# Optimization experiments

Hardware: AMD Instinct MI355X
Metric: run time of the kernel (lower is better)

The kernel has to match this reference:

```python
import jax, jax.numpy as jnp
import numpy as np

DIM = 512
H = 8
HS = DIM // H
SCALES = [25, 12, 7]
ATTN_SCALE = HS ** -0.5
EPS = 1e-5


def _ln(x, g, b):
    m = jnp.mean(x, axis=-1, keepdims=True)
    v = jnp.mean((x - m) ** 2, axis=-1, keepdims=True)
    return (x - m) * jax.lax.rsqrt(v + EPS) * g + b


def setup_inputs() -> dict:
    key = jax.random.key(0)
    ks = jax.random.split(key, 12)
    B, T, J, C = 64, 64, 25, DIM
    w = lambda k, s: jax.random.normal(k, s, dtype=jnp.float32) * 0.02
    return {
        "src": jax.random.normal(ks[0], (B, T, J, C), dtype=jnp.float32),
        "spatial_relation": jax.random.normal(ks[1], (B, T, J, J, 2), dtype=jnp.float32),
        "ln1_g": jnp.ones((C,), jnp.float32),
        "ln1_b": jnp.zeros((C,), jnp.float32),
        "Wq": w(ks[2], (3, C, C)),
        "Wk": w(ks[3], (3, C, C)),
        "Wv": w(ks[4], (3, C, C)),
        "pool0_fc1_w": w(ks[5], (C, 2 * C)),
        "pool0_fc1_b": jnp.zeros((2 * C,), jnp.float32),
        "pool0_fc2_w": w(ks[6], (2 * C, SCALES[1])),
        "pool0_fc2_b": jnp.zeros((SCALES[1],), jnp.float32),
        "pool1_fc1_w": w(ks[7], (C, 2 * C)),
        "pool1_fc1_b": jnp.zeros((2 * C,), jnp.float32),
        "pool1_fc2_w": w(ks[8], (2 * C, SCALES[2])),
        "pool1_fc2_b": jnp.zeros((SCALES[2],), jnp.float32),
    }


def reference(src, spatial_relation, ln1_g, ln1_b, Wq, Wk, Wv,
              pool0_fc1_w, pool0_fc1_b, pool0_fc2_w, pool0_fc2_b,
              pool1_fc1_w, pool1_fc1_b, pool1_fc2_w, pool1_fc2_b):
    # NOTE: in the original torch module, the relation-bias terms (R_qk, R_conv,
    # attn_R_qurt) and spatial_relation_emb are computed but never added to the
    # attention logits, so they do not affect the output; faithful output math below.
    B, T, J, C = src.shape
    x = src.reshape(B * T, J, C)
    g_feat = x  # global (query) features, stay at J nodes
    l_feat = x  # local (key/value) features, get pooled
    pools = [
        (pool0_fc1_w, pool0_fc1_b, pool0_fc2_w, pool0_fc2_b),
        (pool1_fc1_w, pool1_fc1_b, pool1_fc2_w, pool1_fc2_b),
    ]
    outs = []
    for i in range(len(SCALES)):
        qn = _ln(g_feat, ln1_g, ln1_b)
        kn = _ln(l_feat, ln1_g, ln1_b)
        q = (qn @ Wq[i]).reshape(B * T, J, H, HS)
        k = (kn @ Wk[i]).reshape(B * T, -1, H, HS)
        v = (kn @ Wv[i]).reshape(B * T, -1, H, HS)
        logits = jnp.einsum('bnhd,bmhd->bhnm', q, k) * ATTN_SCALE
        a = jax.nn.softmax(logits, axis=-1)
        o = jnp.einsum('bhnm,bmhd->bnhd', a, v).reshape(B * T, J, C)
        outs.append(g_feat + o)
        if i < len(SCALES) - 1:
            f1w, f1b, f2w, f2b = pools[i]
            h = jax.nn.gelu(l_feat @ f1w + f1b, approximate=False)
            S = jax.nn.softmax(h @ f2w + f2b, axis=-1)  # (BT, Ni, Ni+1)
            l_feat = jnp.einsum('bns,bnc->bsc', S, l_feat)
    return jnp.mean(jnp.stack(outs, axis=-1), axis=-1)
```

## Files before the change

kernel.cpp:

```cpp
#include <hip/hip_runtime.h>

typedef unsigned short u16;
typedef unsigned int   u32;
typedef _Float16 f16;
typedef __attribute__((ext_vector_type(8))) unsigned short u16x8;
typedef __attribute__((ext_vector_type(8))) _Float16 f16x8;
typedef __attribute__((ext_vector_type(4))) float f32x4;

__device__ __forceinline__ u16 f2h(float f) {
  f16 h = (f16)f;
  return __builtin_bit_cast(u16, h);
}
__device__ __forceinline__ float h2f(u16 u) {
  return (float)__builtin_bit_cast(f16, u);
}

__global__ __launch_bounds__(256) void prep_w(const float* __restrict__ Wq,
    const float* __restrict__ Wk, const float* __restrict__ Wv,
    const float* __restrict__ f0, const float* __restrict__ f1,
    u16* __restrict__ wt) {
  int t = blockIdx.x * 256 + threadIdx.x;
  float v;
  if (t < 786432) {
    int i = t >> 18, r = t & 262143, n = r >> 9, k = r & 511;
    v = Wq[(size_t)(i << 18) + k * 512 + n];
  } else if (t < 2359296) {
    int r = t - 786432, i = r >> 19, r2 = r & 524287;
    int n = (r2 >> 9) & 511, k = r2 & 511;
    v = ((r2 >> 18) ? Wv : Wk)[(size_t)(i << 18) + k * 512 + n];
  } else if (t < 2883584) {
    int r = t - 2359296, n = r >> 9, k = r & 511;
    v = f0[(size_t)k * 1024 + n];
  } else {
    int r = t - 2883584, n = r >> 9, k = r & 511;
    v = f1[(size_t)k * 1024 + n];
  }
  wt[t] = f2h(v);
}

__global__ __launch_bounds__(256) void ln_f32(const float* __restrict__ x,
    const float* __restrict__ g, const float* __restrict__ bta,
    u16* __restrict__ xn, u16* __restrict__ xb) {
  int row = (blockIdx.x << 2) + (threadIdx.x >> 6);
  int lane = threadIdx.x & 63;
  const float* xr = x + (size_t)row * 512 + (lane << 3);
  float4 a = *(const float4*)xr;
  float4 c = *(const float4*)(xr + 4);
  float v[8] = {a.x, a.y, a.z, a.w, c.x, c.y, c.z, c.w};
  float s = 0.f, s2 = 0.f;
#pragma unroll
  for (int j = 0; j < 8; ++j) { s += v[j]; s2 += v[j] * v[j]; }
  for (int off = 32; off; off >>= 1) { s += __shfl_xor(s, off); s2 += __shfl_xor(s2, off); }
  float mean = s * (1.f / 512.f);
  float var = s2 * (1.f / 512.f) - mean * mean;
  float rs = rsqrtf(var + 1e-5f);
  const float* gp = g + (lane << 3);
  const float* bp = bta + (lane << 3);
  u16x8 pb, pn;
#pragma unroll
  for (int j = 0; j < 8; ++j) {
    pb[j] = f2h(v[j]);
    pn[j] = f2h((v[j] - mean) * rs * gp[j] + bp[j]);
  }
  *(u16x8*)(xb + (size_t)row * 512 + (lane << 3)) = pb;
  *(u16x8*)(xn + (size_t)row * 512 + (lane << 3)) = pn;
}

__global__ __launch_bounds__(256) void ln_b16(const u16* __restrict__ xin,
    const float* __restrict__ g, const float* __restrict__ bta,
    u16* __restrict__ xout) {
  int row = (blockIdx.x << 2) + (threadIdx.x >> 6);
  int lane = threadIdx.x & 63;
  f16x8 u = *(const f16x8*)(xin + (size_t)row * 512 + (lane << 3));
  float v[8];
#pragma unroll
  for (int j = 0; j < 8; ++j) v[j] = (float)u[j];
  float s = 0.f, s2 = 0.f;
#pragma unroll
  for (int j = 0; j < 8; ++j) { s += v[j]; s2 += v[j] * v[j]; }
  for (int off = 32; off; off >>= 1) { s += __shfl_xor(s, off); s2 += __shfl_xor(s2, off); }
  float mean = s * (1.f / 512.f);
  float var = s2 * (1.f / 512.f) - mean * mean;
  float rs = rsqrtf(var + 1e-5f);
  const float* gp = g + (lane << 3);
  const float* bp = bta + (lane << 3);
  u16x8 pn;
#pragma unroll
  for (int j = 0; j < 8; ++j) pn[j] = f2h((v[j] - mean) * rs * gp[j] + bp[j]);
  *(u16x8*)(xout + (size_t)row * 512 + (lane << 3)) = pn;
}

template <bool GELU>
__global__ __launch_bounds__(256, 2) void gemm_bt(const u16* __restrict__ A,
    const u16* __restrict__ Bt, u16* __restrict__ C,
    const float* __restrict__ bias, int M, int N) {
  __shared__ __align__(16) u16 As[128 * 64];
  __shared__ __align__(16) u16 Bs[128 * 64];
  int tid = threadIdx.x;
  int w = tid >> 6, lane = tid & 63;
  int m0 = blockIdx.y << 7, n0 = blockIdx.x << 7;
  int wm = (w & 1) << 6, wn = (w >> 1) << 6;
  f32x4 acc[4][4] = {};
  const int r_off = lane >> 3;
  const int k_off = (lane & 7) << 3;
  for (int kt = 0; kt < 8; ++kt) {
    __syncthreads();
#pragma unroll
    for (int j = 0; j < 4; ++j) {
      int q = (w << 2) + j;
      const u16* gA = A + (size_t)(m0 + (q << 3) + r_off) * 512 + (kt << 6) + k_off;
      __builtin_amdgcn_global_load_lds(
          (const __attribute__((address_space(1))) u32*)gA,
          (__attribute__((address_space(3))) u32*)(As + (q << 9)), 16, 0, 0);
      const u16* gB = Bt + (size_t)(n0 + (q << 3) + r_off) * 512 + (kt << 6) + k_off;
      __builtin_amdgcn_global_load_lds(
          (const __attribute__((address_space(1))) u32*)gB,
          (__attribute__((address_space(3))) u32*)(Bs + (q << 9)), 16, 0, 0);
    }
    asm volatile("s_waitcnt vmcnt(0)" ::: "memory");
    __syncthreads();
#pragma unroll
    for (int kk = 0; kk < 2; ++kk) {
      int ko = (kk << 5) + ((lane >> 4) << 3);
      f16x8 af[4], bfr[4];
#pragma unroll
      for (int mi = 0; mi < 4; ++mi)
        af[mi] = *(const f16x8*)(As + (wm + (mi << 4) + (lane & 15)) * 64 + ko);
#pragma unroll
      for (int ni = 0; ni < 4; ++ni)
        bfr[ni] = *(const f16x8*)(Bs + (wn + (ni << 4) + (lane & 15)) * 64 + ko);
#pragma unroll
      for (int mi = 0; mi < 4; ++mi)
#pragma unroll
        for (int ni = 0; ni < 4; ++ni)
          acc[mi][ni] = __builtin_amdgcn_mfma_f32_16x16x32_f16(af[mi], bfr[ni], acc[mi][ni], 0, 0, 0);
    }
  }
  int cr = (lane >> 4) << 2, cc = lane & 15;
#pragma unroll
  for (int mi = 0; mi < 4; ++mi) {
#pragma unroll
    for (int ni = 0; ni < 4; ++ni) {
      int col = n0 + wn + (ni << 4) + cc;
      float bv = 0.f;
      if (GELU) bv = bias[col];
#pragma unroll
      for (int j = 0; j < 4; ++j) {
        int row = m0 + wm + (mi << 4) + cr + j;
        float v = acc[mi][ni][j];
        if (GELU) { v += bv; v = 0.5f * v * (1.f + erff(v * 0.70710678118f)); }
        C[(size_t)row * N + col] = f2h(v);
      }
    }
  }
}

template <int NKV, bool INIT, int MINW>
__global__ __launch_bounds__(512, MINW) void attn(const u16* __restrict__ Q,
    const u16* __restrict__ KV, const u16* __restrict__ xb, float* __restrict__ out) {
  constexpr int G = 8;
  constexpr int ELEMS = NKV * 1024;
  __shared__ __align__(16) u16 KVl[2][ELEMS];
  int tid = threadIdx.x;
  int b0 = blockIdx.x * G;
  int h = tid >> 6, r = tid & 63, n = r >> 1, half = r & 1;
  int dbase = (h << 6) + (half << 5);
  {
    const u16* src = KV + (size_t)b0 * ELEMS;
    for (int e = tid * 8; e < ELEMS; e += 4096)
      __builtin_amdgcn_global_load_lds(
          (const __attribute__((address_space(1))) u32*)(src + e),
          (__attribute__((address_space(3))) u32*)(KVl[0] + e), 16, 0, 0);
  }
  asm volatile("s_waitcnt vmcnt(0)" ::: "memory");
  __syncthreads();
  for (int t = 0; t < G; ++t) {
    const u16* KVc = KVl[t & 1];
    if (t + 1 < G) {
      const u16* src = KV + (size_t)(b0 + t + 1) * ELEMS;
      u16* dst = KVl[(t + 1) & 1];
      for (int e = tid * 8; e < ELEMS; e += 4096)
        __builtin_amdgcn_global_load_lds(
            (const __attribute__((address_space(1))) u32*)(src + e),
            (__attribute__((address_space(3))) u32*)(dst + e), 16, 0, 0);
    }
    int b = b0 + t;
    if (n < 25) {
      const u16* qr = Q + (size_t)(b * 25 + n) * 512 + dbase;
      f16x8 q8[4];
#pragma unroll
      for (int i = 0; i < 4; ++i) q8[i] = *(const f16x8*)(qr + (i << 3));
      float s[NKV];
      float mx = -1e30f;
#pragma unroll
      for (int m = 0; m < NKV; ++m) {
        const u16* kr = KVc + m * 1024 + dbase;
        float p = 0.f;
#pragma unroll
        for (int i = 0; i < 4; ++i) {
          f16x8 kv = *(const f16x8*)(kr + (i << 3));
#pragma unroll
          for (int j = 0; j < 8; ++j) p += (float)q8[i][j] * (float)kv[j];
        }
        float d = p + __shfl_xor(p, 1);
        s[m] = d * 0.125f;
        mx = fmaxf(mx, s[m]);
      }
      float sum = 0.f;
#pragma unroll
      for (int m = 0; m < NKV; ++m) { s[m] = __expf(s[m] - mx); sum += s[m]; }
      float o[32] = {};
#pragma unroll
      for (int m = 0; m < NKV; ++m) {
        float a = s[m];
        const u16* vr = KVc + m * 1024 + 512 + dbase;
#pragma unroll
        for (int i = 0; i < 4; ++i) {
          f16x8 vv = *(const f16x8*)(vr + (i << 3));
#pragma unroll
          for (int j = 0; j < 8; ++j) o[i * 8 + j] += a * (float)vv[j];
        }
      }
      float sc = (1.f / sum) * (1.f / 3.f);
      float* orow = out + (size_t)(b * 25 + n) * 512 + dbase;
      if (INIT) {
        const u16* xrow = xb + (size_t)(b * 25 + n) * 512 + dbase;
#pragma unroll
        for (int i = 0; i < 4; ++i) {
          f16x8 xv = *(const f16x8*)(xrow + (i << 3));
#pragma unroll
          for (int j = 0; j < 8; j += 4) {
            float4 rr;
            rr.x = o[i * 8 + j + 0] * sc + (float)xv[j + 0];
            rr.y = o[i * 8 + j + 1] * sc + (float)xv[j + 1];
            rr.z = o[i * 8 + j + 2] * sc + (float)xv[j + 2];
            rr.w = o[i * 8 + j + 3] * sc + (float)xv[j + 3];
            *(float4*)(orow + i * 8 + j) = rr;
          }
        }
      } else {
#pragma unroll
        for (int i = 0; i < 8; ++i) {
          float4 pv = *(const float4*)(orow + i * 4);
          float4 rr;
          rr.x = o[i * 4 + 0] * sc + pv.x;
          rr.y = o[i * 4 + 1] * sc + pv.y;
          rr.z = o[i * 4 + 2] * sc + pv.z;
          rr.w = o[i * 4 + 3] * sc + pv.w;
          *(float4*)(orow + i * 4) = rr;
        }
      }
    }
    asm volatile("s_waitcnt vmcnt(0)" ::: "memory");
    __syncthreads();
  }
}

template <int NIN, int NOUT>
__global__ __launch_bounds__(256) void pool(const u16* __restrict__ h,
    const u16* __restrict__ lf, const float* __restrict__ w2,
    const float* __restrict__ b2, u16* __restrict__ lout) {
  __shared__ __align__(16) float W2l[1024 * NOUT];
  __shared__ __align__(16) u16 Xl[NIN * 512];
  __shared__ __align__(16) float Sl[NIN * NOUT];
  int b = blockIdx.x, tid = threadIdx.x;
  for (int e = tid; e < 1024 * NOUT; e += 256) W2l[e] = w2[e];
  for (int e = tid * 8; e < NIN * 512; e += 2048)
    *(u16x8*)(Xl + e) = *(const u16x8*)(lf + (size_t)b * NIN * 512 + e);
  __syncthreads();
  if (tid < NIN * 8) {
    int nn = tid >> 3, sub = tid & 7;
    float p[NOUT] = {};
    const u16* hr = h + (size_t)(b * NIN + nn) * 1024;
    for (int cc = 0; cc < 128; ++cc) {
      int c = sub + (cc << 3);
      float hv = h2f(hr[c]);
#pragma unroll
      for (int s2 = 0; s2 < NOUT; ++s2) p[s2] += hv * W2l[c * NOUT + s2];
    }
#pragma unroll
    for (int s2 = 0; s2 < NOUT; ++s2) {
      p[s2] += __shfl_down(p[s2], 4, 8);
      p[s2] += __shfl_down(p[s2], 2, 8);
      p[s2] += __shfl_down(p[s2], 1, 8);
    }
    if (sub == 0) {
      float mx = -1e30f;
#pragma unroll
      for (int s2 = 0; s2 < NOUT; ++s2) { p[s2] += b2[s2]; mx = fmaxf(mx, p[s2]); }
      float sum = 0.f;
#pragma unroll
      for (int s2 = 0; s2 < NOUT; ++s2) { p[s2] = __expf(p[s2] - mx); sum += p[s2]; }
      float inv = 1.f / sum;
#pragma unroll
      for (int s2 = 0; s2 < NOUT; ++s2) Sl[nn * NOUT + s2] = p[s2] * inv;
    }
  }
  __syncthreads();
  int c0 = tid << 1;
#pragma unroll
  for (int s2 = 0; s2 < NOUT; ++s2) {
    float a0 = 0.f, a1 = 0.f;
#pragma unroll
    for (int nn = 0; nn < NIN; ++nn) {
      float wv = Sl[nn * NOUT + s2];
      a0 += wv * h2f(Xl[nn * 512 + c0]);
      a1 += wv * h2f(Xl[nn * 512 + c0 + 1]);
    }
    u32 pk = (u32)f2h(a0) | ((u32)f2h(a1) << 16);
    *(u32*)(lout + (size_t)(b * NOUT + s2) * 512 + c0) = pk;
  }
}

extern "C" void kernel_launch(void* const* d_in, const int* in_sizes, int n_in,
                              void* d_out, int out_size, void* d_ws, size_t ws_size,
                              hipStream_t stream) {
  const float* src = (const float*)d_in[0];
  const float* g    = (const float*)d_in[2];
  const float* bt   = (const float*)d_in[3];
  const float* Wq   = (const float*)d_in[4];
  const float* Wk   = (const float*)d_in[5];
  const float* Wv   = (const float*)d_in[6];
  const float* f0w  = (const float*)d_in[7];
  const float* f0b  = (const float*)d_in[8];
  const float* f0w2 = (const float*)d_in[9];
  const float* f0b2 = (const float*)d_in[10];
  const float* f1w  = (const float*)d_in[11];
  const float* f1b  = (const float*)d_in[12];
  const float* f1w2 = (const float*)d_in[13];
  const float* f1b2 = (const float*)d_in[14];
  float* out = (float*)d_out;
  char* ws = (char*)d_ws;

  u16* wt  = (u16*)(ws + 0);
  u16* xn  = (u16*)(ws + 6815744);
  u16* xb  = (u16*)(ws + 111673344);
  u16* qb  = (u16*)(ws + 216530944);
  u16* B1  = (u16*)(ws + 321388544);
  u16* l1  = (u16*)(ws + 426246144);
  u16* kn1 = (u16*)(ws + 476577792);
  u16* l2  = qb;
  u16* kn2 = qb + 14680064;

  prep_w<<<13312, 256, 0, stream>>>(Wq, Wk, Wv, f0w, f1w, wt);
  ln_f32<<<25600, 256, 0, stream>>>(src, g, bt, xn, xb);

  gemm_bt<false><<<dim3(4, 800), 256, 0, stream>>>(xn, wt, qb, nullptr, 102400, 512);
  for (int s = 0; s < 2; ++s) {
    size_t ro = (size_t)s * 51200;
    gemm_bt<false><<<dim3(8, 400), 256, 0, stream>>>(xn + ro * 512, wt + 786432, B1, nullptr, 51200, 1024);
    attn<25, true, 1><<<256, 512, 0, stream>>>(qb + ro * 512, B1, xb + ro * 512, out + ro * 512);
  }

  for (int s = 0; s < 2; ++s) {
    size_t ro = (size_t)s * 51200;
    gemm_bt<true><<<dim3(8, 400), 256, 0, stream>>>(xb + ro * 512, wt + 2359296, B1, f0b, 51200, 1024);
    pool<25, 12><<<2048, 256, 0, stream>>>(B1, xb + ro * 512, f0w2, f0b2, l1 + (size_t)s * 2048 * 12 * 512);
  }
  ln_b16<<<12288, 256, 0, stream>>>(l1, g, bt, kn1);

  gemm_bt<false><<<dim3(4, 800), 256, 0, stream>>>(xn, wt + 262144, qb, nullptr, 102400, 512);
  gemm_bt<false><<<dim3(8, 384), 256, 0, stream>>>(kn1, wt + 786432 + 524288, B1, nullptr, 49152, 1024);
  attn<12, false, 2><<<512, 512, 0, stream>>>(qb, B1, nullptr, out);

  gemm_bt<true><<<dim3(8, 384), 256, 0, stream>>>(l1, wt + 2883584, B1, f1b, 49152, 1024);
  pool<12, 7><<<4096, 256, 0, stream>>>(B1, l1, f1w2, f1b2, l2);
  ln_b16<<<7168, 256, 0, stream>>>(l2, g, bt, kn2);

  gemm_bt<false><<<dim3(8, 224), 256, 0, stream>>>(kn2, wt + 786432 + 1048576, B1, nullptr, 28672, 1024);
  gemm_bt<false><<<dim3(4, 800), 256, 0, stream>>>(xn, wt + 524288, qb, nullptr, 102400, 512);
  attn<7, false, 2><<<512, 512, 0, stream>>>(qb, B1, nullptr, out);
}
```

Before: 1.773 ms.

## Use packed fp16 math in attention, fp16 partial sums, swizzle GEMM tiles

The attention QK dot products and PV accumulation now use packed half-precision vector math instead of per-element fp32 FMAs. When the workspace is large enough, the per-scale attention partial sums go to an fp16 scratch buffer rather than a read-modify-write of the fp32 output, and the last scale combines them with the residual into fp32. The GEMM remaps block indices with a swizzle so neighbouring workgroups spread across the grid, which may change cache locality. Accumulating in fp16 cuts ALU and memory traffic but risks lower accuracy.

```diff
diff --git a/kernel.cpp b/kernel.cpp
--- a/kernel.cpp
+++ b/kernel.cpp
@@ -5,6 +5,7 @@
 typedef _Float16 f16;
 typedef __attribute__((ext_vector_type(8))) unsigned short u16x8;
 typedef __attribute__((ext_vector_type(8))) _Float16 f16x8;
+typedef __attribute__((ext_vector_type(2))) _Float16 f16x2;
 typedef __attribute__((ext_vector_type(4))) float f32x4;
 
 __device__ __forceinline__ u16 f2h(float f) {
@@ -98,7 +99,10 @@
   __shared__ __align__(16) u16 Bs[128 * 64];
   int tid = threadIdx.x;
   int w = tid >> 6, lane = tid & 63;
-  int m0 = blockIdx.y << 7, n0 = blockIdx.x << 7;
+  int nwg = gridDim.x * gridDim.y;
+  int wg = blockIdx.x + gridDim.x * blockIdx.y;
+  int swz = (wg & 7) * (nwg >> 3) + (wg >> 3);
+  int m0 = (swz / gridDim.x) << 7, n0 = (swz % gridDim.x) << 7;
   int wm = (w & 1) << 6, wn = (w >> 1) << 6;
   f32x4 acc[4][4] = {};
   const int r_off = lane >> 3;
@@ -155,9 +159,10 @@
   }
 }
 
-template <int NKV, bool INIT, int MINW>
+template <int NKV, int PMODE, int MINW>
 __global__ __launch_bounds__(512, MINW) void attn(const u16* __restrict__ Q,
-    const u16* __restrict__ KV, const u16* __restrict__ xb, float* __restrict__ out) {
+    const u16* __restrict__ KV, const u16* __restrict__ xb,
+    float* __restrict__ out, u16* __restrict__ p) {
   constexpr int G = 8;
   constexpr int ELEMS = NKV * 1024;
   __shared__ __align__(16) u16 KVl[2][ELEMS];
@@ -190,64 +195,105 @@
       f16x8 q8[4];
 #pragma unroll
       for (int i = 0; i < 4; ++i) q8[i] = *(const f16x8*)(qr + (i << 3));
+      const f16x2* q2 = (const f16x2*)q8;
       float s[NKV];
       float mx = -1e30f;
 #pragma unroll
       for (int m = 0; m < NKV; ++m) {
         const u16* kr = KVc + m * 1024 + dbase;
-        float p = 0.f;
+        f16x2 a0 = {(f16)0.f, (f16)0.f}, a1 = a0;
 #pragma unroll
         for (int i = 0; i < 4; ++i) {
           f16x8 kv = *(const f16x8*)(kr + (i << 3));
-#pragma unroll
-          for (int j = 0; j < 8; ++j) p += (float)q8[i][j] * (float)kv[j];
+          const f16x2* k2 = (const f16x2*)&kv;
+          a0 += q2[i * 4 + 0] * k2[0];
+          a1 += q2[i * 4 + 1] * k2[1];
+          a0 += q2[i * 4 + 2] * k2[2];
+          a1 += q2[i * 4 + 3] * k2[3];
         }
-        float d = p + __shfl_xor(p, 1);
+        f16x2 at = a0 + a1;
+        float d = (float)at[0] + (float)at[1];
+        d += __shfl_xor(d, 1);
         s[m] = d * 0.125f;
         mx = fmaxf(mx, s[m]);
       }
       float sum = 0.f;
 #pragma unroll
       for (int m = 0; m < NKV; ++m) { s[m] = __expf(s[m] - mx); sum += s[m]; }
-      float o[32] = {};
+      f16x8 o8[4] = {};
 #pragma unroll
       for (int m = 0; m < NKV; ++m) {
-        float a = s[m];
+        f16 ah = (f16)s[m];
+        f16x8 av = {ah, ah, ah, ah, ah, ah, ah, ah};
         const u16* vr = KVc + m * 1024 + 512 + dbase;
 #pragma unroll
         for (int i = 0; i < 4; ++i) {
           f16x8 vv = *(const f16x8*)(vr + (i << 3));
-#pragma unroll
-          for (int j = 0; j < 8; ++j) o[i * 8 + j] += a * (float)vv[j];
+          o8[i] += vv * av;
         }
       }
-      float sc = (1.f / sum) * (1.f / 3.f);
-      float* orow = out + (size_t)(b * 25 + n) * 512 + dbase;
-      if (INIT) {
-        const u16* xrow = xb + (size_t)(b * 25 + n) * 512 + dbase;
+      size_t rowoff = (size_t)(b * 25 + n) * 512 + dbase;
+      if (PMODE == 0 || PMODE == 1) {
+        float sc = (1.f / sum) * (1.f / 3.f);
+        float* orow = out + rowoff;
+        const u16* xrow = xb + rowoff;
 #pragma unroll
         for (int i = 0; i < 4; ++i) {
-          f16x8 xv = *(const f16x8*)(xrow + (i << 3));
+          f16x8 xv;
+          if (PMODE == 0) xv = *(const f16x8*)(xrow + (i << 3));
 #pragma unroll
           for (int j = 0; j < 8; j += 4) {
             float4 rr;
-            rr.x = o[i * 8 + j + 0] * sc + (float)xv[j + 0];
-            rr.y = o[i * 8 + j + 1] * sc + (float)xv[j + 1];
-            rr.z = o[i * 8 + j + 2] * sc + (float)xv[j + 2];
-            rr.w = o[i * 8 + j + 3] * sc + (float)xv[j + 3];
-            *(float4*)(orow + i * 8 + j) = rr;
+            if (PMODE == 0) {
+              rr.x = (float)o8[i][j + 0] * sc + (float)xv[j + 0];
+              rr.y = (float)o8[i][j + 1] * sc + (float)xv[j + 1];
+              rr.z = (float)o8[i][j + 2] * sc + (float)xv[j + 2];
+              rr.w = (float)o8[i][j + 3] * sc + (float)xv[j + 3];
+            } else {
+              float4 pv = *(const float4*)(orow + (i << 3) + j);
+              rr.x = (float)o8[i][j + 0] * sc + pv.x;
+              rr.y = (float)o8[i][j + 1] * sc + pv.y;
+              rr.z = (float)o8[i][j + 2] * sc + pv.z;
+              rr.w = (float)o8[i][j + 3] * sc + pv.w;
+            }
+            *(float4*)(orow + (i << 3) + j) = rr;
           }
         }
+      } else if (PMODE == 2 || PMODE == 3) {
+        float sc = 1.f / sum;
+        u16* prow = p + rowoff;
+#pragma unroll
+        for (int i = 0; i < 4; ++i) {
+          u16x8 pk;
+          if (PMODE == 3) {
+            f16x8 pv = *(const f16x8*)(prow + (i << 3));
+#pragma unroll
+            for (int j = 0; j < 8; ++j)
+              pk[j] = f2h((float)o8[i][j] * sc + (float)pv[j]);
+          } else {
+#pragma unroll
+            for (int j = 0; j < 8; ++j) pk[j] = f2h((float)o8[i][j] * sc);
+          }
+          *(u16x8*)(prow + (i << 3)) = pk;
+        }
       } else {
-#pragma unroll
-        for (int i = 0; i < 8; ++i) {
-          float4 pv = *(const float4*)(orow + i * 4);
-          float4 rr;
-          rr.x = o[i * 4 + 0] * sc + pv.x;
-          rr.y = o[i * 4 + 1] * sc + pv.y;
-          rr.z = o[i * 4 + 2] * sc + pv.z;
-          rr.w = o[i * 4 + 3] * sc + pv.w;
-          *(float4*)(orow + i * 4) = rr;
+        float sc = 1.f / sum;
+        float* orow = out + rowoff;
+        const u16* prow = p + rowoff;
+        const u16* xrow = xb + rowoff;
+#pragma unroll
+        for (int i = 0; i < 4; ++i) {
+          f16x8 pv = *(const f16x8*)(prow + (i << 3));
+          f16x8 xv = *(const f16x8*)(xrow + (i << 3));
+#pragma unroll
+          for (int j = 0; j < 8; j += 4) {
+            float4 rr;
+            rr.x = (float)xv[j + 0] + ((float)pv[j + 0] + (float)o8[i][j + 0] * sc) * (1.f / 3.f);
+            rr.y = (float)xv[j + 1] + ((float)pv[j + 1] + (float)o8[i][j + 1] * sc) * (1.f / 3.f);
+            rr.z = (float)xv[j + 2] + ((float)pv[j + 2] + (float)o8[i][j + 2] * sc) * (1.f / 3.f);
+            rr.w = (float)xv[j + 3] + ((float)pv[j + 3] + (float)o8[i][j + 3] * sc) * (1.f / 3.f);
+            *(float4*)(orow + (i << 3) + j) = rr;
+          }
         }
       }
     }
@@ -270,30 +316,30 @@
   __syncthreads();
   if (tid < NIN * 8) {
     int nn = tid >> 3, sub = tid & 7;
-    float p[NOUT] = {};
+    float pl[NOUT] = {};
     const u16* hr = h + (size_t)(b * NIN + nn) * 1024;
     for (int cc = 0; cc < 128; ++cc) {
       int c = sub + (cc << 3);
       float hv = h2f(hr[c]);
 #pragma unroll
-      for (int s2 = 0; s2 < NOUT; ++s2) p[s2] += hv * W2l[c * NOUT + s2];
+      for (int s2 = 0; s2 < NOUT; ++s2) pl[s2] += hv * W2l[c * NOUT + s2];
     }
 #pragma unroll
     for (int s2 = 0; s2 < NOUT; ++s2) {
-      p[s2] += __shfl_down(p[s2], 4, 8);
-      p[s2] += __shfl_down(p[s2], 2, 8);
-      p[s2] += __shfl_down(p[s2], 1, 8);
+      pl[s2] += __shfl_down(pl[s2], 4, 8);
+      pl[s2] += __shfl_down(pl[s2], 2, 8);
+      pl[s2] += __shfl_down(pl[s2], 1, 8);
     }
     if (sub == 0) {
       float mx = -1e30f;
 #pragma unroll
-      for (int s2 = 0; s2 < NOUT; ++s2) { p[s2] += b2[s2]; mx = fmaxf(mx, p[s2]); }
+      for (int s2 = 0; s2 < NOUT; ++s2) { pl[s2] += b2[s2]; mx = fmaxf(mx, pl[s2]); }
       float sum = 0.f;
 #pragma unroll
-      for (int s2 = 0; s2 < NOUT; ++s2) { p[s2] = __expf(p[s2] - mx); sum += p[s2]; }
+      for (int s2 = 0; s2 < NOUT; ++s2) { pl[s2] = __expf(pl[s2] - mx); sum += pl[s2]; }
       float inv = 1.f / sum;
 #pragma unroll
-      for (int s2 = 0; s2 < NOUT; ++s2) Sl[nn * NOUT + s2] = p[s2] * inv;
+      for (int s2 = 0; s2 < NOUT; ++s2) Sl[nn * NOUT + s2] = pl[s2] * inv;
     }
   }
   __syncthreads();
@@ -341,6 +387,8 @@
   u16* kn1 = (u16*)(ws + 476577792);
   u16* l2  = qb;
   u16* kn2 = qb + 14680064;
+  bool bigws = ws_size >= 640000000ull;
+  u16* pbuf = (u16*)(ws + 526909440);
 
   prep_w<<<13312, 256, 0, stream>>>(Wq, Wk, Wv, f0w, f1w, wt);
   ln_f32<<<25600, 256, 0, stream>>>(src, g, bt, xn, xb);
@@ -349,7 +397,10 @@
   for (int s = 0; s < 2; ++s) {
     size_t ro = (size_t)s * 51200;
     gemm_bt<false><<<dim3(8, 400), 256, 0, stream>>>(xn + ro * 512, wt + 786432, B1, nullptr, 51200, 1024);
-    attn<25, true, 1><<<256, 512, 0, stream>>>(qb + ro * 512, B1, xb + ro * 512, out + ro * 512);
+    if (bigws)
+      attn<25, 2, 1><<<256, 512, 0, stream>>>(qb + ro * 512, B1, xb + ro * 512, out + ro * 512, pbuf + ro * 512);
+    else
+      attn<25, 0, 1><<<256, 512, 0, stream>>>(qb + ro * 512, B1, xb + ro * 512, out + ro * 512, pbuf);
   }
 
   for (int s = 0; s < 2; ++s) {
@@ -361,7 +412,10 @@
 
   gemm_bt<false><<<dim3(4, 800), 256, 0, stream>>>(xn, wt + 262144, qb, nullptr, 102400, 512);
   gemm_bt<false><<<dim3(8, 384), 256, 0, stream>>>(kn1, wt + 786432 + 524288, B1, nullptr, 49152, 1024);
-  attn<12, false, 2><<<512, 512, 0, stream>>>(qb, B1, nullptr, out);
+  if (bigws)
+    attn<12, 3, 2><<<512, 512, 0, stream>>>(qb, B1, xb, out, pbuf);
+  else
+    attn<12, 1, 2><<<512, 512, 0, stream>>>(qb, B1, xb, out, pbuf);
 
   gemm_bt<true><<<dim3(8, 384), 256, 0, stream>>>(l1, wt + 2883584, B1, f1b, 49152, 1024);
   pool<12, 7><<<4096, 256, 0, stream>>>(B1, l1, f1w2, f1b2, l2);
@@ -369,5 +423,8 @@
 
   gemm_bt<false><<<dim3(8, 224), 256, 0, stream>>>(kn2, wt + 786432 + 1048576, B1, nullptr, 28672, 1024);
   gemm_bt<false><<<dim3(4, 800), 256, 0, stream>>>(xn, wt + 524288, qb, nullptr, 102400, 512);
-  attn<7, false, 2><<<512, 512, 0, stream>>>(qb, B1, nullptr, out);
-}
+  if (bigws)
+    attn<7, 4, 2><<<512, 512, 0, stream>>>(qb, B1, xb, out, pbuf);
+  else
+    attn<7, 1, 2><<<512, 512, 0, stream>>>(qb, B1, xb, out, pbuf);
+}
```

Result: faster. 1.569 ms (-11.5%).
